# Performance work log

Measured on AMD Instinct MI355X. Metric: run time of the kernel, lower is better.

## Reference

```python
import jax, jax.numpy as jnp
import numpy as np
from jax import lax

WIN_SIZE = 11
WIN_SIGMA = 1.5
LEVELS = 5


def _gauss_win(size, sigma):
    coords = jnp.arange(size, dtype=jnp.float32) - size // 2
    g = jnp.exp(-(coords * coords) / (2.0 * sigma * sigma))
    return g / jnp.sum(g)


def _gaussian_filter(x, win):
    # separable depthwise gaussian blur, VALID padding (as in pytorch-msssim)
    C = x.shape[1]
    kh = jnp.tile(win.reshape(1, 1, -1, 1), (C, 1, 1, 1))  # (C,1,K,1)
    kw = jnp.tile(win.reshape(1, 1, 1, -1), (C, 1, 1, 1))  # (C,1,1,K)
    dn = ('NCHW', 'OIHW', 'NCHW')
    x = lax.conv_general_dilated(x, kh, (1, 1), 'VALID', feature_group_count=C, dimension_numbers=dn)
    x = lax.conv_general_dilated(x, kw, (1, 1), 'VALID', feature_group_count=C, dimension_numbers=dn)
    return x


def _ssim(X, Y, win, data_range=1.0):
    K1, K2 = 0.01, 0.03
    C1 = (K1 * data_range) ** 2
    C2 = (K2 * data_range) ** 2
    mu1 = _gaussian_filter(X, win)
    mu2 = _gaussian_filter(Y, win)
    mu1_sq = mu1 * mu1
    mu2_sq = mu2 * mu2
    mu12 = mu1 * mu2
    sigma1_sq = _gaussian_filter(X * X, win) - mu1_sq
    sigma2_sq = _gaussian_filter(Y * Y, win) - mu2_sq
    sigma12 = _gaussian_filter(X * Y, win) - mu12
    cs_map = (2.0 * sigma12 + C2) / (sigma1_sq + sigma2_sq + C2)
    ssim_map = ((2.0 * mu12 + C1) / (mu1_sq + mu2_sq + C1)) * cs_map
    return ssim_map.mean(axis=(2, 3)), cs_map.mean(axis=(2, 3))  # (N,C) each


def _avg_pool2(x):
    # kernel 2, stride 2, count_include_pad=True, pad if odd (matches F.avg_pool2d usage)
    N, C, H, W = x.shape
    ph, pw = H % 2, W % 2
    if ph or pw:
        x = jnp.pad(x, ((0, 0), (0, 0), (ph, ph), (pw, pw)))
    s = lax.reduce_window(x, 0.0, lax.add, (1, 1, 2, 2), (1, 1, 2, 2), 'VALID')
    return s * 0.25


def _ms_ssim(X, Y):
    win = _gauss_win(WIN_SIZE, WIN_SIGMA).astype(X.dtype)
    weights = jnp.array([0.0448, 0.2856, 0.3001, 0.2363, 0.1333], dtype=X.dtype)
    mcs = []
    for i in range(LEVELS):
        ssim_pc, cs = _ssim(X, Y, win, data_range=1.0)
        if i < LEVELS - 1:
            mcs.append(jax.nn.relu(cs))
            X = _avg_pool2(X)
            Y = _avg_pool2(Y)
    vals = jnp.stack(mcs + [jax.nn.relu(ssim_pc)])  # (L, N, C)
    ms = jnp.prod(vals ** weights[:, None, None], axis=0)  # (N, C)
    return jnp.mean(ms)  # size_average=True


def setup_inputs() -> dict:
    key = jax.random.key(0)
    k1, k2 = jax.random.split(key)
    output = jax.random.uniform(k1, (32, 3, 512, 512), dtype=jnp.float32)
    target = jax.random.uniform(k2, (32, 3, 512, 512), dtype=jnp.float32)
    return {"output": output, "target": target}


def reference(output, target):
    return 1.0 - _ms_ssim(output, target)
```

## Files before the change

### kernel.cpp

```cpp
#include <hip/hip_runtime.h>
#include <math.h>


struct GWin { float w[11]; };

__global__ __launch_bounds__(256)
void ssim_rows_kernel(const float* __restrict__ X, const float* __restrict__ Y,
                      float* __restrict__ poolX, float* __restrict__ poolY,
                      float* __restrict__ accum,
                      int S, int outS, int doPool, int rps, int tpcLog, GWin gw)
{
    __shared__ float4 ab[2][2][264];

    const int tid = threadIdx.x;
    const int tpc = 1 << tpcLog;
    const int lt  = tid & (tpc - 1);
    const int sub = tid >> tpcLog;
    const int ch  = blockIdx.z * (256 >> tpcLog) + sub;
    const int oy0 = blockIdx.x * rps;
    const int halfS = S >> 1;
    const int gc  = 2 * lt;

    int rowsOut = outS - oy0; if (rowsOut > rps) rowsOut = rps;
    const int NIT = (rowsOut + 11) >> 1;

    const float* Xc = X + (size_t)ch * S * S;
    const float* Yc = Y + (size_t)ch * S * S;

    float2 sx0, sy0, sx1, sy1;

    auto issue = [&](int baseRow) {
        int gr0 = baseRow;     if (gr0 > S - 1) gr0 = S - 1;
        int gr1 = baseRow + 1; if (gr1 > S - 1) gr1 = S - 1;
        sx0 = *reinterpret_cast<const float2*>(Xc + (size_t)gr0 * S + gc);
        sy0 = *reinterpret_cast<const float2*>(Yc + (size_t)gr0 * S + gc);
        sx1 = *reinterpret_cast<const float2*>(Xc + (size_t)gr1 * S + gc);
        sy1 = *reinterpret_cast<const float2*>(Yc + (size_t)gr1 * S + gc);
    };
    auto write_slot = [&](int sl) {
        ab[sl][0][tid] = make_float4(sx0.x + sy0.x, sx0.x - sy0.x,
                                     sx0.y + sy0.y, sx0.y - sy0.y);
        ab[sl][1][tid] = make_float4(sx1.x + sy1.x, sx1.x - sy1.x,
                                     sx1.y + sy1.y, sx1.y - sy1.y);
    };

    float pendP[2][12], pendQ[2][12], pendU[2][12], pendV[2][12];
    #pragma unroll
    for (int c = 0; c < 2; ++c)
        #pragma unroll
        for (int j = 0; j < 12; ++j) { pendP[c][j] = 0.f; pendQ[c][j] = 0.f; pendU[c][j] = 0.f; pendV[c][j] = 0.f; }

    float ssum = 0.f, csum = 0.f;
    const float C1x2 = 2e-4f, C2x2 = 1.8e-3f;
    const bool ok0 = (gc    ) < outS;
    const bool ok1 = (gc + 1) < outS;

    if (tid < 8) {
        float4 z = make_float4(0.f, 0.f, 0.f, 0.f);
        ab[0][0][256 + tid] = z; ab[0][1][256 + tid] = z;
        ab[1][0][256 + tid] = z; ab[1][1][256 + tid] = z;
    }
    issue(oy0);
    write_slot(0);
    issue(oy0 + 2);
    __syncthreads();

    for (int k = 0; k < NIT; ++k) {
        const int sl = k & 1;

        float hP[2][2], hQ[2][2], hU[2][2], hV[2][2];
        float4 u0save[2];
        #pragma unroll
        for (int r = 0; r < 2; ++r) {
            const float4* bp = &ab[sl][r][tid];
            float4 u[6];
            #pragma unroll
            for (int i = 0; i < 6; ++i) u[i] = bp[i];
            u0save[r] = u[0];
            const float* v = reinterpret_cast<const float*>(u);
            float sqa[12], sqb[12];
            #pragma unroll
            for (int j = 0; j < 12; ++j) {
                float a = v[2 * j], b = v[2 * j + 1];
                sqa[j] = a * a; sqb[j] = b * b;
            }
            float P0 = 0.f, Q0 = 0.f, U0 = 0.f, V0 = 0.f;
            float P1 = 0.f, Q1 = 0.f, U1 = 0.f, V1 = 0.f;
            #pragma unroll
            for (int t = 0; t < 11; ++t) {
                float wt = gw.w[t];
                P0 = fmaf(wt, v[2 * t],     P0);
                Q0 = fmaf(wt, v[2 * t + 1], Q0);
                U0 = fmaf(wt, sqa[t],       U0);
                V0 = fmaf(wt, sqb[t],       V0);
                P1 = fmaf(wt, v[2 * t + 2], P1);
                Q1 = fmaf(wt, v[2 * t + 3], Q1);
                U1 = fmaf(wt, sqa[t + 1],   U1);
                V1 = fmaf(wt, sqb[t + 1],   V1);
            }
            hP[r][0] = P0; hQ[r][0] = Q0; hU[r][0] = U0; hV[r][0] = V0;
            hP[r][1] = P1; hQ[r][1] = Q1; hU[r][1] = U1; hV[r][1] = V1;
        }

        #pragma unroll
        for (int c = 0; c < 2; ++c) {
            #pragma unroll
            for (int j = 0; j <= 10; ++j) {
                float wt = gw.w[10 - j];
                pendP[c][j] = fmaf(wt, hP[0][c], pendP[c][j]);
                pendQ[c][j] = fmaf(wt, hQ[0][c], pendQ[c][j]);
                pendU[c][j] = fmaf(wt, hU[0][c], pendU[c][j]);
                pendV[c][j] = fmaf(wt, hV[0][c], pendV[c][j]);
            }
            #pragma unroll
            for (int j = 1; j <= 11; ++j) {
                float wt = gw.w[11 - j];
                pendP[c][j] = fmaf(wt, hP[1][c], pendP[c][j]);
                pendQ[c][j] = fmaf(wt, hQ[1][c], pendQ[c][j]);
                pendU[c][j] = fmaf(wt, hU[1][c], pendU[c][j]);
                pendV[c][j] = fmaf(wt, hV[1][c], pendV[c][j]);
            }
        }

        #pragma unroll
        for (int e = 0; e < 2; ++e) {
            int rel = 2 * k - 10 + e;
            bool rowok = (unsigned)rel < (unsigned)rowsOut;
            #pragma unroll
            for (int c = 0; c < 2; ++c) {
                float p = pendP[c][e], q = pendQ[c][e];
                float uu = pendU[c][e], vv = pendV[c][e];
                float p2 = p * p, q2 = q * q;
                float A = p2 - q2;
                float csn = (uu - vv - A) + C2x2;
                float csd = (uu + vv - p2 - q2) + C2x2;
                float cs  = csn * __builtin_amdgcn_rcpf(csd);
                float ss  = (A + C1x2) * __builtin_amdgcn_rcpf(p2 + q2 + C1x2) * cs;
                if (rowok && (c ? ok1 : ok0)) { ssum += ss; csum += cs; }
            }
        }

        #pragma unroll
        for (int c = 0; c < 2; ++c) {
            #pragma unroll
            for (int j = 0; j < 10; ++j) {
                pendP[c][j] = pendP[c][j + 2]; pendQ[c][j] = pendQ[c][j + 2];
                pendU[c][j] = pendU[c][j + 2]; pendV[c][j] = pendV[c][j + 2];
            }
            pendP[c][10] = 0.f; pendP[c][11] = 0.f;
            pendQ[c][10] = 0.f; pendQ[c][11] = 0.f;
            pendU[c][10] = 0.f; pendU[c][11] = 0.f;
            pendV[c][10] = 0.f; pendV[c][11] = 0.f;
        }

        if (doPool && k < (rps >> 1)) {
            float sa = u0save[0].x + u0save[0].z + u0save[1].x + u0save[1].z;
            float sb = u0save[0].y + u0save[0].w + u0save[1].y + u0save[1].w;
            int prow = (oy0 >> 1) + k;
            size_t o = (size_t)ch * halfS * halfS + (size_t)prow * halfS + lt;
            poolX[o] = 0.125f * (sa + sb);
            poolY[o] = 0.125f * (sa - sb);
        }

        if (k + 1 < NIT) {
            write_slot(sl ^ 1);
            if (k + 2 < NIT) issue(oy0 + 2 * (k + 2));
        }
        __syncthreads();
    }

    {
        int rw = (tpc < 64) ? tpc : 64;
        for (int off = rw >> 1; off > 0; off >>= 1) {
            ssum += __shfl_down(ssum, off);
            csum += __shfl_down(csum, off);
        }
        if ((lt & 63) == 0) {
            atomicAdd(&accum[ch], ssum);
            atomicAdd(&accum[96 + ch], csum);
        }
    }
}

__global__ __launch_bounds__(256)
void pool_pyramid_kernel(const float* __restrict__ p1x, const float* __restrict__ p1y,
                         float* __restrict__ p2x, float* __restrict__ p2y,
                         float* __restrict__ p3x, float* __restrict__ p3y,
                         float* __restrict__ p4x, float* __restrict__ p4y)
{
    const int tid  = threadIdx.x;
    const int ch   = blockIdx.y;
    const int tile = blockIdx.x;
    const int ty0 = (tile >> 2) * 64, tx0 = (tile & 3) * 64;
    const int tr = tid >> 4, tc = tid & 15;
    const int iy = ty0 + 4 * tr, ix = tx0 + 4 * tc;

    const float* X1 = p1x + (size_t)ch * 256 * 256;
    const float* Y1 = p1y + (size_t)ch * 256 * 256;

    float4 xr[4], yr[4];
    #pragma unroll
    for (int r = 0; r < 4; ++r) {
        xr[r] = *reinterpret_cast<const float4*>(X1 + (size_t)(iy + r) * 256 + ix);
        yr[r] = *reinterpret_cast<const float4*>(Y1 + (size_t)(iy + r) * 256 + ix);
    }

    float x200 = 0.25f * (xr[0].x + xr[0].y + xr[1].x + xr[1].y);
    float x201 = 0.25f * (xr[0].z + xr[0].w + xr[1].z + xr[1].w);
    float x210 = 0.25f * (xr[2].x + xr[2].y + xr[3].x + xr[3].y);
    float x211 = 0.25f * (xr[2].z + xr[2].w + xr[3].z + xr[3].w);
    float y200 = 0.25f * (yr[0].x + yr[0].y + yr[1].x + yr[1].y);
    float y201 = 0.25f * (yr[0].z + yr[0].w + yr[1].z + yr[1].w);
    float y210 = 0.25f * (yr[2].x + yr[2].y + yr[3].x + yr[3].y);
    float y211 = 0.25f * (yr[2].z + yr[2].w + yr[3].z + yr[3].w);
    {
        int oy = iy >> 1, ox = ix >> 1;
        float* bx = p2x + (size_t)ch * 128 * 128;
        float* by = p2y + (size_t)ch * 128 * 128;
        *reinterpret_cast<float2*>(bx + (size_t)oy * 128 + ox)       = make_float2(x200, x201);
        *reinterpret_cast<float2*>(bx + (size_t)(oy + 1) * 128 + ox) = make_float2(x210, x211);
        *reinterpret_cast<float2*>(by + (size_t)oy * 128 + ox)       = make_float2(y200, y201);
        *reinterpret_cast<float2*>(by + (size_t)(oy + 1) * 128 + ox) = make_float2(y210, y211);
    }

    float x3 = 0.25f * (x200 + x201 + x210 + x211);
    float y3 = 0.25f * (y200 + y201 + y210 + y211);
    p3x[(size_t)ch * 64 * 64 + (size_t)(iy >> 2) * 64 + (ix >> 2)] = x3;
    p3y[(size_t)ch * 64 * 64 + (size_t)(iy >> 2) * 64 + (ix >> 2)] = y3;

    float x4 = x3 + __shfl_xor(x3, 1);
    float y4 = y3 + __shfl_xor(y3, 1);
    x4 += __shfl_xor(x4, 16);
    y4 += __shfl_xor(y4, 16);
    if (((tr | tc) & 1) == 0) {
        p4x[(size_t)ch * 32 * 32 + (size_t)(iy >> 3) * 32 + (ix >> 3)] = 0.25f * x4;
        p4y[(size_t)ch * 32 * 32 + (size_t)(iy >> 3) * 32 + (ix >> 3)] = 0.25f * y4;
    }
}

__global__ __launch_bounds__(256)
void ssim_rest_kernel(const float* __restrict__ x1, const float* __restrict__ y1,
                      const float* __restrict__ x2, const float* __restrict__ y2,
                      const float* __restrict__ x3, const float* __restrict__ y3,
                      const float* __restrict__ x4, const float* __restrict__ y4,
                      float* __restrict__ accum, GWin gw)
{
    __shared__ float4 ab[2][2][264];

    const int bid = blockIdx.x;
    const int L = (bid >= 624) ? 3 : (bid >= 576) ? 2 : (bid >= 384) ? 1 : 0;
    const int off0 = (L == 0) ? 0 : (L == 1) ? 384 : (L == 2) ? 576 : 624;
    const int r = bid - off0;

    const int S      = (L == 0) ? 256 : (L == 1) ? 128 : (L == 2) ? 64 : 32;
    const int outS   = (L == 0) ? 246 : (L == 1) ? 118 : (L == 2) ? 54 : 22;
    const int rps    = (L == 0) ? 32  : (L == 1) ? 16  : (L == 2) ? 16 : 22;
    const int tpcLog = (L == 0) ? 7   : (L == 1) ? 6   : (L == 2) ? 5  : 4;
    const int stripsLog = (L == 0) ? 3 : (L == 1) ? 3 : (L == 2) ? 2 : 0;
    const float* Xl = (L == 0) ? x1 : (L == 1) ? x2 : (L == 2) ? x3 : x4;
    const float* Yl = (L == 0) ? y1 : (L == 1) ? y2 : (L == 2) ? y3 : y4;
    float* acc = accum + 192 * (L + 1);

    const int zidx  = r >> stripsLog;
    const int strip = r & ((1 << stripsLog) - 1);

    const int tid = threadIdx.x;
    const int tpc = 1 << tpcLog;
    const int lt  = tid & (tpc - 1);
    const int sub = tid >> tpcLog;
    const int ch  = zidx * (256 >> tpcLog) + sub;
    const int oy0 = strip * rps;
    const int gc  = 2 * lt;

    int rowsOut = outS - oy0; if (rowsOut > rps) rowsOut = rps;
    const int NIT = (rowsOut + 11) >> 1;

    const float* Xc = Xl + (size_t)ch * S * S;
    const float* Yc = Yl + (size_t)ch * S * S;

    float2 sx0, sy0, sx1, sy1;

    auto issue = [&](int baseRow) {
        int gr0 = baseRow;     if (gr0 > S - 1) gr0 = S - 1;
        int gr1 = baseRow + 1; if (gr1 > S - 1) gr1 = S - 1;
        sx0 = *reinterpret_cast<const float2*>(Xc + (size_t)gr0 * S + gc);
        sy0 = *reinterpret_cast<const float2*>(Yc + (size_t)gr0 * S + gc);
        sx1 = *reinterpret_cast<const float2*>(Xc + (size_t)gr1 * S + gc);
        sy1 = *reinterpret_cast<const float2*>(Yc + (size_t)gr1 * S + gc);
    };
    auto write_slot = [&](int sl) {
        ab[sl][0][tid] = make_float4(sx0.x + sy0.x, sx0.x - sy0.x,
                                     sx0.y + sy0.y, sx0.y - sy0.y);
        ab[sl][1][tid] = make_float4(sx1.x + sy1.x, sx1.x - sy1.x,
                                     sx1.y + sy1.y, sx1.y - sy1.y);
    };

    float pendP[2][12], pendQ[2][12], pendU[2][12], pendV[2][12];
    #pragma unroll
    for (int c = 0; c < 2; ++c)
        #pragma unroll
        for (int j = 0; j < 12; ++j) { pendP[c][j] = 0.f; pendQ[c][j] = 0.f; pendU[c][j] = 0.f; pendV[c][j] = 0.f; }

    float ssum = 0.f, csum = 0.f;
    const float C1x2 = 2e-4f, C2x2 = 1.8e-3f;
    const bool ok0 = gc < outS, ok1 = (gc + 1) < outS;

    if (tid < 8) {
        float4 z = make_float4(0.f, 0.f, 0.f, 0.f);
        ab[0][0][256 + tid] = z; ab[0][1][256 + tid] = z;
        ab[1][0][256 + tid] = z; ab[1][1][256 + tid] = z;
    }
    issue(oy0);
    write_slot(0);
    issue(oy0 + 2);
    __syncthreads();

    for (int k = 0; k < NIT; ++k) {
        const int sl = k & 1;

        float hP[2][2], hQ[2][2], hU[2][2], hV[2][2];
        #pragma unroll
        for (int r2 = 0; r2 < 2; ++r2) {
            const float4* bp = &ab[sl][r2][tid];
            float4 u[6];
            #pragma unroll
            for (int i = 0; i < 6; ++i) u[i] = bp[i];
            const float* v = reinterpret_cast<const float*>(u);
            float sqa[12], sqb[12];
            #pragma unroll
            for (int j = 0; j < 12; ++j) {
                float a = v[2 * j], b = v[2 * j + 1];
                sqa[j] = a * a; sqb[j] = b * b;
            }
            float P0 = 0.f, Q0 = 0.f, U0 = 0.f, V0 = 0.f;
            float P1 = 0.f, Q1 = 0.f, U1 = 0.f, V1 = 0.f;
            #pragma unroll
            for (int t = 0; t < 11; ++t) {
                float wt = gw.w[t];
                P0 = fmaf(wt, v[2 * t],     P0);
                Q0 = fmaf(wt, v[2 * t + 1], Q0);
                U0 = fmaf(wt, sqa[t],       U0);
                V0 = fmaf(wt, sqb[t],       V0);
                P1 = fmaf(wt, v[2 * t + 2], P1);
                Q1 = fmaf(wt, v[2 * t + 3], Q1);
                U1 = fmaf(wt, sqa[t + 1],   U1);
                V1 = fmaf(wt, sqb[t + 1],   V1);
            }
            hP[r2][0] = P0; hQ[r2][0] = Q0; hU[r2][0] = U0; hV[r2][0] = V0;
            hP[r2][1] = P1; hQ[r2][1] = Q1; hU[r2][1] = U1; hV[r2][1] = V1;
        }

        #pragma unroll
        for (int c = 0; c < 2; ++c) {
            #pragma unroll
            for (int j = 0; j <= 10; ++j) {
                float wt = gw.w[10 - j];
                pendP[c][j] = fmaf(wt, hP[0][c], pendP[c][j]);
                pendQ[c][j] = fmaf(wt, hQ[0][c], pendQ[c][j]);
                pendU[c][j] = fmaf(wt, hU[0][c], pendU[c][j]);
                pendV[c][j] = fmaf(wt, hV[0][c], pendV[c][j]);
            }
            #pragma unroll
            for (int j = 1; j <= 11; ++j) {
                float wt = gw.w[11 - j];
                pendP[c][j] = fmaf(wt, hP[1][c], pendP[c][j]);
                pendQ[c][j] = fmaf(wt, hQ[1][c], pendQ[c][j]);
                pendU[c][j] = fmaf(wt, hU[1][c], pendU[c][j]);
                pendV[c][j] = fmaf(wt, hV[1][c], pendV[c][j]);
            }
        }

        #pragma unroll
        for (int e = 0; e < 2; ++e) {
            int rel = 2 * k - 10 + e;
            bool rowok = (unsigned)rel < (unsigned)rowsOut;
            #pragma unroll
            for (int c = 0; c < 2; ++c) {
                float p = pendP[c][e], q = pendQ[c][e];
                float uu = pendU[c][e], vv = pendV[c][e];
                float p2 = p * p, q2 = q * q;
                float A = p2 - q2;
                float csn = (uu - vv - A) + C2x2;
                float csd = (uu + vv - p2 - q2) + C2x2;
                float cs  = csn * __builtin_amdgcn_rcpf(csd);
                float ss  = (A + C1x2) * __builtin_amdgcn_rcpf(p2 + q2 + C1x2) * cs;
                if (rowok && (c ? ok1 : ok0)) { ssum += ss; csum += cs; }
            }
        }

        #pragma unroll
        for (int c = 0; c < 2; ++c) {
            #pragma unroll
            for (int j = 0; j < 10; ++j) {
                pendP[c][j] = pendP[c][j + 2]; pendQ[c][j] = pendQ[c][j + 2];
                pendU[c][j] = pendU[c][j + 2]; pendV[c][j] = pendV[c][j + 2];
            }
            pendP[c][10] = 0.f; pendP[c][11] = 0.f;
            pendQ[c][10] = 0.f; pendQ[c][11] = 0.f;
            pendU[c][10] = 0.f; pendU[c][11] = 0.f;
            pendV[c][10] = 0.f; pendV[c][11] = 0.f;
        }

        if (k + 1 < NIT) {
            write_slot(sl ^ 1);
            if (k + 2 < NIT) issue(oy0 + 2 * (k + 2));
        }
        __syncthreads();
    }

    {
        int rw = (tpc < 64) ? tpc : 64;
        for (int off = rw >> 1; off > 0; off >>= 1) {
            ssum += __shfl_down(ssum, off);
            csum += __shfl_down(csum, off);
        }
        if ((lt & 63) == 0) {
            atomicAdd(&acc[ch], ssum);
            atomicAdd(&acc[96 + ch], csum);
        }
    }
}

__global__ void finalize_kernel(const float* __restrict__ accum, float* __restrict__ out)
{
    __shared__ float red[2];
    const int t = threadIdx.x;
    const float w[5]   = {0.0448f, 0.2856f, 0.3001f, 0.2363f, 0.1333f};
    const float inv[5] = {1.f / (502.f * 502.f), 1.f / (246.f * 246.f),
                          1.f / (118.f * 118.f), 1.f / (54.f * 54.f),
                          1.f / (22.f * 22.f)};
    float ms = 0.f;
    if (t < 96) {
        ms = 1.f;
        #pragma unroll
        for (int l = 0; l < 5; ++l) {
            float v = (l < 4) ? accum[l * 192 + 96 + t] : accum[l * 192 + t];
            v *= inv[l];
            v = fmaxf(v, 0.f);
            ms *= powf(v, w[l]);
        }
    }
    for (int off = 32; off > 0; off >>= 1) ms += __shfl_down(ms, off);
    int wid = t >> 6, lane = t & 63;
    if (lane == 0) red[wid] = ms;
    __syncthreads();
    if (t == 0) out[0] = 1.f - (red[0] + red[1]) * (1.f / 96.f);
}

extern "C" void kernel_launch(void* const* d_in, const int* in_sizes, int n_in,
                              void* d_out, int out_size, void* d_ws, size_t ws_size,
                              hipStream_t stream)
{
    (void)in_sizes; (void)n_in; (void)out_size; (void)ws_size;
    const float* X = (const float*)d_in[0];
    const float* Y = (const float*)d_in[1];
    float* out = (float*)d_out;
    float* ws  = (float*)d_ws;

    GWin gw;
    {
        double g[11], s = 0.0;
        for (int i = 0; i < 11; ++i) { double d = i - 5; g[i] = exp(-(d * d) / 4.5); s += g[i]; }
        for (int i = 0; i < 11; ++i) gw.w[i] = (float)(g[i] / s);
    }

    float* accum = ws;
    size_t off = 1024;
    float* p1x = ws + off; off += (size_t)96 * 256 * 256;
    float* p1y = ws + off; off += (size_t)96 * 256 * 256;
    float* p2x = ws + off; off += (size_t)96 * 128 * 128;
    float* p2y = ws + off; off += (size_t)96 * 128 * 128;
    float* p3x = ws + off; off += (size_t)96 * 64 * 64;
    float* p3y = ws + off; off += (size_t)96 * 64 * 64;
    float* p4x = ws + off; off += (size_t)96 * 32 * 32;
    float* p4y = ws + off; off += (size_t)96 * 32 * 32;

    hipMemsetAsync(accum, 0, 5 * 192 * sizeof(float), stream);

    ssim_rows_kernel<<<dim3(8, 1, 96), 256, 0, stream>>>(
        X, Y, p1x, p1y, accum, 512, 502, 1, 64, 8, gw);

    pool_pyramid_kernel<<<dim3(16, 96), 256, 0, stream>>>(
        p1x, p1y, p2x, p2y, p3x, p3y, p4x, p4y);

    ssim_rest_kernel<<<dim3(630), 256, 0, stream>>>(
        p1x, p1y, p2x, p2y, p3x, p3y, p4x, p4y, accum, gw);

    finalize_kernel<<<1, 128, 0, stream>>>(accum, out);
}
```

Baseline: 150.2 us.

## Give each wavefront its own column strip with halo to drop block barriers

The level-0 SSIM kernel now splits each 512-wide row into four 128-column strips, one per wavefront. Each wavefront loads its own 10-column halo into a private LDS region, so the per-iteration __syncthreads and the zero-padding setup are removed. Sizes are hardcoded for the 512x512 input. In exchange, halo columns are loaded redundantly, and correctness now relies on lockstep execution within a wavefront for LDS ordering.

```diff
diff --git a/kernel.cpp b/kernel.cpp
--- a/kernel.cpp
+++ b/kernel.cpp
@@ -5,43 +5,52 @@
 struct GWin { float w[11]; };
 
 __global__ __launch_bounds__(256)
-void ssim_rows_kernel(const float* __restrict__ X, const float* __restrict__ Y,
-                      float* __restrict__ poolX, float* __restrict__ poolY,
-                      float* __restrict__ accum,
-                      int S, int outS, int doPool, int rps, int tpcLog, GWin gw)
+void ssim_l0_kernel(const float* __restrict__ X, const float* __restrict__ Y,
+                    float* __restrict__ p1x, float* __restrict__ p1y,
+                    float* __restrict__ accum, GWin gw)
 {
-    __shared__ float4 ab[2][2][264];
+    const int S = 512, outS = 502;
+    __shared__ float4 ab[4][2][2][70];
 
     const int tid = threadIdx.x;
-    const int tpc = 1 << tpcLog;
-    const int lt  = tid & (tpc - 1);
-    const int sub = tid >> tpcLog;
-    const int ch  = blockIdx.z * (256 >> tpcLog) + sub;
-    const int oy0 = blockIdx.x * rps;
-    const int halfS = S >> 1;
-    const int gc  = 2 * lt;
-
-    int rowsOut = outS - oy0; if (rowsOut > rps) rowsOut = rps;
+    const int w   = tid >> 6;
+    const int ln  = tid & 63;
+    const int ch  = blockIdx.z;
+    const int oy0 = blockIdx.x * 64;
+    const int gxb = 128 * w;
+    const int gc  = gxb + 2 * ln;
+
+    int rowsOut = outS - oy0; if (rowsOut > 64) rowsOut = 64;
     const int NIT = (rowsOut + 11) >> 1;
 
     const float* Xc = X + (size_t)ch * S * S;
     const float* Yc = Y + (size_t)ch * S * S;
 
-    float2 sx0, sy0, sx1, sy1;
-
+    const int  r1_ = (ln >= 5) ? 1 : 0;
+    const int  u1_ = (ln >= 5) ? (ln - 5) : (ln + 64);
+    const bool hasT2 = (ln < 10);
+    const int  u2_ = 59 + ln;
+
+    float2 sx0, sy0, sx1, sy1, sx2, sy2;
+
+    auto ld1 = [&](int baseRow, int rr, int uu, float2& xo, float2& yo) {
+        int gr = baseRow + rr; if (gr > S - 1) gr = S - 1;
+        int gcol = gxb + 2 * uu; if (gcol > S - 2) gcol = S - 2;
+        xo = *reinterpret_cast<const float2*>(Xc + (size_t)gr * S + gcol);
+        yo = *reinterpret_cast<const float2*>(Yc + (size_t)gr * S + gcol);
+    };
     auto issue = [&](int baseRow) {
-        int gr0 = baseRow;     if (gr0 > S - 1) gr0 = S - 1;
-        int gr1 = baseRow + 1; if (gr1 > S - 1) gr1 = S - 1;
-        sx0 = *reinterpret_cast<const float2*>(Xc + (size_t)gr0 * S + gc);
-        sy0 = *reinterpret_cast<const float2*>(Yc + (size_t)gr0 * S + gc);
-        sx1 = *reinterpret_cast<const float2*>(Xc + (size_t)gr1 * S + gc);
-        sy1 = *reinterpret_cast<const float2*>(Yc + (size_t)gr1 * S + gc);
+        ld1(baseRow, 0,   ln,  sx0, sy0);
+        ld1(baseRow, r1_, u1_, sx1, sy1);
+        if (hasT2) ld1(baseRow, 1, u2_, sx2, sy2);
+    };
+    auto pack = [](float2 x, float2 y) {
+        return make_float4(x.x + y.x, x.x - y.x, x.y + y.y, x.y - y.y);
     };
     auto write_slot = [&](int sl) {
-        ab[sl][0][tid] = make_float4(sx0.x + sy0.x, sx0.x - sy0.x,
-                                     sx0.y + sy0.y, sx0.y - sy0.y);
-        ab[sl][1][tid] = make_float4(sx1.x + sy1.x, sx1.x - sy1.x,
-                                     sx1.y + sy1.y, sx1.y - sy1.y);
+        ab[w][sl][0][ln]    = pack(sx0, sy0);
+        ab[w][sl][r1_][u1_] = pack(sx1, sy1);
+        if (hasT2) ab[w][sl][1][u2_] = pack(sx2, sy2);
     };
 
     float pendP[2][12], pendQ[2][12], pendU[2][12], pendV[2][12];
@@ -55,15 +64,9 @@
     const bool ok0 = (gc    ) < outS;
     const bool ok1 = (gc + 1) < outS;
 
-    if (tid < 8) {
-        float4 z = make_float4(0.f, 0.f, 0.f, 0.f);
-        ab[0][0][256 + tid] = z; ab[0][1][256 + tid] = z;
-        ab[1][0][256 + tid] = z; ab[1][1][256 + tid] = z;
-    }
     issue(oy0);
     write_slot(0);
     issue(oy0 + 2);
-    __syncthreads();
 
     for (int k = 0; k < NIT; ++k) {
         const int sl = k & 1;
@@ -72,7 +75,7 @@
         float4 u0save[2];
         #pragma unroll
         for (int r = 0; r < 2; ++r) {
-            const float4* bp = &ab[sl][r][tid];
+            const float4* bp = &ab[w][sl][r][ln];
             float4 u[6];
             #pragma unroll
             for (int i = 0; i < 6; ++i) u[i] = bp[i];
@@ -153,32 +156,28 @@
             pendV[c][10] = 0.f; pendV[c][11] = 0.f;
         }
 
-        if (doPool && k < (rps >> 1)) {
+        if (k < 32) {
             float sa = u0save[0].x + u0save[0].z + u0save[1].x + u0save[1].z;
             float sb = u0save[0].y + u0save[0].w + u0save[1].y + u0save[1].w;
             int prow = (oy0 >> 1) + k;
-            size_t o = (size_t)ch * halfS * halfS + (size_t)prow * halfS + lt;
-            poolX[o] = 0.125f * (sa + sb);
-            poolY[o] = 0.125f * (sa - sb);
+            size_t o = (size_t)ch * 256 * 256 + (size_t)prow * 256 + 64 * w + ln;
+            p1x[o] = 0.125f * (sa + sb);
+            p1y[o] = 0.125f * (sa - sb);
         }
 
         if (k + 1 < NIT) {
             write_slot(sl ^ 1);
             if (k + 2 < NIT) issue(oy0 + 2 * (k + 2));
         }
-        __syncthreads();
-    }
-
-    {
-        int rw = (tpc < 64) ? tpc : 64;
-        for (int off = rw >> 1; off > 0; off >>= 1) {
-            ssum += __shfl_down(ssum, off);
-            csum += __shfl_down(csum, off);
-        }
-        if ((lt & 63) == 0) {
-            atomicAdd(&accum[ch], ssum);
-            atomicAdd(&accum[96 + ch], csum);
-        }
+    }
+
+    for (int off = 32; off > 0; off >>= 1) {
+        ssum += __shfl_down(ssum, off);
+        csum += __shfl_down(csum, off);
+    }
+    if (ln == 0) {
+        atomicAdd(&accum[ch], ssum);
+        atomicAdd(&accum[96 + ch], csum);
     }
 }
 
@@ -477,8 +476,8 @@
 
     hipMemsetAsync(accum, 0, 5 * 192 * sizeof(float), stream);
 
-    ssim_rows_kernel<<<dim3(8, 1, 96), 256, 0, stream>>>(
-        X, Y, p1x, p1y, accum, 512, 502, 1, 64, 8, gw);
+    ssim_l0_kernel<<<dim3(8, 1, 96), 256, 0, stream>>>(
+        X, Y, p1x, p1y, accum, gw);
 
     pool_pyramid_kernel<<<dim3(16, 96), 256, 0, stream>>>(
         p1x, p1y, p2x, p2y, p3x, p3y, p4x, p4y);
```

Result: slower. 156.9 us (+4.4%).
